# Performance work log

Measured on AMD Instinct MI355X. Metric: run time of the kernel, lower is better.

Reference implementation:

```python
import jax, jax.numpy as jnp
import numpy as np

B, P, E, H, V, T = 128, 196, 512, 512, 12000, 20  # batch, pixels, embed, hidden, vocab, timesteps


def setup_inputs() -> dict:
    key = jax.random.key(0)
    ks = jax.random.split(key, 12)
    s = lambda k, shape: jax.random.normal(k, shape, jnp.float32) * 0.02
    return {
        "encoder_out": jax.random.normal(ks[0], (B, P, E), jnp.float32),
        "captions": jax.random.randint(ks[1], (B, T), 0, V),
        "emb_table": s(ks[2], (V, E)),
        "We_att": s(ks[3], (E, E)), "be_att": jnp.zeros((E,), jnp.float32),
        "Wd_att": s(ks[4], (E, H)), "bd_att": jnp.zeros((E,), jnp.float32),
        "Wf_att": s(ks[5], (1, E)), "bf_att": jnp.zeros((1,), jnp.float32),
        "W_ih": s(ks[6], (4 * H, 2 * E)), "b_ih": jnp.zeros((4 * H,), jnp.float32),
        "W_hh": s(ks[7], (4 * H, H)), "b_hh": jnp.zeros((4 * H,), jnp.float32),
        "W_beta": s(ks[8], (E, H)), "b_beta": jnp.zeros((E,), jnp.float32),
        "W_fc": s(ks[9], (V, H)), "b_fc": jnp.zeros((V,), jnp.float32),
    }


def reference(encoder_out, captions, emb_table, We_att, be_att, Wd_att, bd_att,
              Wf_att, bf_att, W_ih, b_ih, W_hh, b_hh, W_beta, b_beta, W_fc, b_fc):
    # Dropout in eval mode (identity) for a deterministic reference.
    Bv = encoder_out.shape[0]
    Hd = W_hh.shape[1]
    emb = emb_table[captions]                                   # [B,T,E]
    # loop-invariant encoder projection (cached across timesteps)
    att1 = jnp.einsum('bpe,ae->bpa', encoder_out, We_att) + be_att  # [B,P,A]

    def step(carry, emb_t):
        h, c = carry
        att2 = h @ Wd_att.T + bd_att                            # [B,A]
        att = jax.nn.relu(att1 + att2[:, None, :])              # [B,P,A]
        e = jnp.einsum('bpa,a->bp', att, Wf_att[0]) + bf_att[0] # [B,P]
        alpha = jax.nn.softmax(e, axis=1)
        ctx = jnp.einsum('bp,bpe->be', alpha, encoder_out)      # [B,E]
        x = jnp.concatenate([emb_t, ctx], axis=1)               # [B,2E]
        gates = x @ W_ih.T + b_ih + h @ W_hh.T + b_hh           # [B,4H]
        i, f, g, o = jnp.split(gates, 4, axis=1)
        c = jax.nn.sigmoid(f) * c + jax.nn.sigmoid(i) * jnp.tanh(g)
        h = jax.nn.sigmoid(o) * jnp.tanh(c)
        gate = jax.nn.sigmoid(h @ W_beta.T + b_beta)            # [B,E]
        out = (gate * h) @ W_fc.T + b_fc                        # [B,V]
        return (h, c), (out, alpha)

    h0 = jnp.zeros((Bv, Hd), encoder_out.dtype)
    c0 = jnp.zeros((Bv, Hd), encoder_out.dtype)
    _, (outs, alphas) = jax.lax.scan(step, (h0, c0), jnp.swapaxes(emb, 0, 1))
    return jnp.swapaxes(outs, 0, 1), jnp.swapaxes(alphas, 0, 1)
```

## Files before the change

### kernel.cpp

```cpp
#include <hip/hip_runtime.h>
#include <math.h>

#define Bv 128
#define Pv 196
#define Ev 512
#define Hv 512
#define Vv 12000
#define Tv 20

typedef unsigned short u16;
typedef unsigned int u32;
typedef short bf16x8 __attribute__((ext_vector_type(8)));
typedef float f32x4 __attribute__((ext_vector_type(4)));

__device__ __forceinline__ float sigf(float x) { return 1.0f / (1.0f + __expf(-x)); }
__device__ __forceinline__ u16 f2bf(float f) {
    u32 x = __float_as_uint(f);
    return (u16)((x + 0x7FFFu + ((x >> 16) & 1u)) >> 16);
}
__device__ __forceinline__ u32 pack2(float a, float b) {
    return (u32)f2bf(a) | ((u32)f2bf(b) << 16);
}
__device__ __forceinline__ float bfl(u32 u) { return __uint_as_float(u << 16); }
__device__ __forceinline__ float bfh(u32 u) { return __uint_as_float(u & 0xFFFF0000u); }
__device__ __forceinline__ float bf2f(u16 u) { return __uint_as_float(((u32)u) << 16); }

__global__ __launch_bounds__(256) void k_cvt(const float* __restrict__ src,
                                             u16* __restrict__ dst, int n4) {
    for (int i = blockIdx.x * 256 + threadIdx.x; i < n4; i += gridDim.x * 256) {
        float4 v = ((const float4*)src)[i];
        uint2 o;
        o.x = pack2(v.x, v.y);
        o.y = pack2(v.z, v.w);
        ((uint2*)dst)[i] = o;
    }
}


__global__ __launch_bounds__(256) void k_att1_mfma(const u16* __restrict__ A,
                                                   const u16* __restrict__ Bw,
                                                   const float* __restrict__ bias,
                                                   u16* __restrict__ C) {
    __shared__ u16 As[128][72];
    __shared__ u16 Bs[64][72];
    const int n0 = blockIdx.x * 64;
    const int m0 = blockIdx.y * 128;
    const int tid = threadIdx.x;
    const int lane = tid & 63, wid = tid >> 6;
    const int wm = wid >> 1, wn = wid & 1;
    f32x4 acc[4][2] = {};
    for (int kt = 0; kt < 8; kt++) {
#pragma unroll
        for (int p = 0; p < 4; p++) {
            int flat = p * 256 + tid, row = flat >> 3, ch = flat & 7;
            *(uint4*)&As[row][ch * 8] = *(const uint4*)&A[(size_t)(m0 + row) * 512 + kt * 64 + ch * 8];
        }
#pragma unroll
        for (int p = 0; p < 2; p++) {
            int flat = p * 256 + tid, row = flat >> 3, ch = flat & 7;
            *(uint4*)&Bs[row][ch * 8] = *(const uint4*)&Bw[(size_t)(n0 + row) * 512 + kt * 64 + ch * 8];
        }
        __syncthreads();
#pragma unroll
        for (int ks = 0; ks < 2; ks++) {
            int kk = ks * 32 + (lane >> 4) * 8;
            bf16x8 af[4], bfr[2];
#pragma unroll
            for (int mf = 0; mf < 4; mf++) af[mf] = *(const bf16x8*)&As[wm * 64 + mf * 16 + (lane & 15)][kk];
#pragma unroll
            for (int nf = 0; nf < 2; nf++) bfr[nf] = *(const bf16x8*)&Bs[wn * 32 + nf * 16 + (lane & 15)][kk];
#pragma unroll
            for (int mf = 0; mf < 4; mf++)
#pragma unroll
                for (int nf = 0; nf < 2; nf++)
                    acc[mf][nf] = __builtin_amdgcn_mfma_f32_16x16x32_bf16(af[mf], bfr[nf], acc[mf][nf], 0, 0, 0);
        }
        __syncthreads();
    }
#pragma unroll
    for (int mf = 0; mf < 4; mf++)
#pragma unroll
        for (int nf = 0; nf < 2; nf++)
#pragma unroll
            for (int r = 0; r < 4; r++) {
                int m = m0 + wm * 64 + mf * 16 + (lane >> 4) * 4 + r;
                int n = n0 + wn * 32 + nf * 16 + (lane & 15);
                C[(size_t)m * 512 + n] = f2bf(acc[mf][nf][r] + bias[n]);
            }
}

__global__ __launch_bounds__(512) void k_attn(const u16* __restrict__ att1b,
                                              const u16* __restrict__ encb,
                                              const u16* __restrict__ hprev,
                                              const u16* __restrict__ Wdb,
                                              const float* __restrict__ bd,
                                              const float* __restrict__ Wf,
                                              u16* __restrict__ ctxb,
                                              float* __restrict__ alpha_out,
                                              int t) {
    __shared__ float h_s[512];
    __shared__ float att2_s[512];
    __shared__ float e_s[200];
    __shared__ float alpha_s[200];
    const int b = blockIdx.x;
    const int tid = threadIdx.x;

    h_s[tid] = bf2f(hprev[b * 512 + tid]);
    __syncthreads();

    {
        float acc = bd[tid];
        const uint4* wrow = (const uint4*)&Wdb[(size_t)tid * 512];
        const float4* hv4 = (const float4*)h_s;
#pragma unroll 4
        for (int i = 0; i < 64; i++) {
            uint4 w = wrow[i];
            float4 x0 = hv4[2 * i], x1 = hv4[2 * i + 1];
            acc += bfl(w.x) * x0.x + bfh(w.x) * x0.y + bfl(w.y) * x0.z + bfh(w.y) * x0.w
                 + bfl(w.z) * x1.x + bfh(w.z) * x1.y + bfl(w.w) * x1.z + bfh(w.w) * x1.w;
        }
        att2_s[tid] = acc;
    }
    __syncthreads();

    const int lane = tid & 63;
    const int wv = tid >> 6;
    float att2r[8], wfr[8];
#pragma unroll
    for (int j = 0; j < 8; j++) {
        att2r[j] = att2_s[lane * 8 + j];
        wfr[j] = Wf[lane * 8 + j];
    }
    for (int p = wv; p < 196; p += 8) {
        uint4 q = *(const uint4*)&att1b[((size_t)(b * 196 + p)) * 512 + lane * 8];
        float s = wfr[0] * fmaxf(bfl(q.x) + att2r[0], 0.f) + wfr[1] * fmaxf(bfh(q.x) + att2r[1], 0.f)
                + wfr[2] * fmaxf(bfl(q.y) + att2r[2], 0.f) + wfr[3] * fmaxf(bfh(q.y) + att2r[3], 0.f)
                + wfr[4] * fmaxf(bfl(q.z) + att2r[4], 0.f) + wfr[5] * fmaxf(bfh(q.z) + att2r[5], 0.f)
                + wfr[6] * fmaxf(bfl(q.w) + att2r[6], 0.f) + wfr[7] * fmaxf(bfh(q.w) + att2r[7], 0.f);
#pragma unroll
        for (int off = 32; off; off >>= 1) s += __shfl_xor(s, off);
        if (lane == 0) e_s[p] = s;
    }
    __syncthreads();

    if (wv == 0) {
        float v0 = e_s[lane], v1 = e_s[lane + 64], v2 = e_s[lane + 128];
        float v3 = (lane < 4) ? e_s[lane + 192] : -1e30f;
        float mx = fmaxf(fmaxf(v0, v1), fmaxf(v2, v3));
#pragma unroll
        for (int off = 32; off; off >>= 1) mx = fmaxf(mx, __shfl_xor(mx, off));
        float x0 = __expf(v0 - mx), x1 = __expf(v1 - mx), x2 = __expf(v2 - mx);
        float x3 = (lane < 4) ? __expf(v3 - mx) : 0.f;
        float sm = x0 + x1 + x2 + x3;
#pragma unroll
        for (int off = 32; off; off >>= 1) sm += __shfl_xor(sm, off);
        float inv = 1.0f / sm;
        x0 *= inv; x1 *= inv; x2 *= inv; x3 *= inv;
        alpha_s[lane] = x0; alpha_s[lane + 64] = x1; alpha_s[lane + 128] = x2;
        if (lane < 4) alpha_s[lane + 192] = x3;
        float* ao = alpha_out + ((size_t)b * Tv + t) * 196;
        ao[lane] = x0; ao[lane + 64] = x1; ao[lane + 128] = x2;
        if (lane < 4) ao[lane + 192] = x3;
    }
    __syncthreads();

    {
        float acc = 0.f;
        const u16* ecol = &encb[(size_t)b * 196 * 512 + tid];
#pragma unroll 4
        for (int p = 0; p < 196; p++) acc += alpha_s[p] * bf2f(ecol[(size_t)p * 512]);
        ctxb[b * 512 + tid] = f2bf(acc);
    }
}

__global__ __launch_bounds__(256) void k_gateslstm(const float* __restrict__ embt,
                                                   const int* __restrict__ caps,
                                                   const u16* __restrict__ ctxb,
                                                   const u16* __restrict__ hprev,
                                                   const u16* __restrict__ Wihb,
                                                   const u16* __restrict__ Whhb,
                                                   const float* __restrict__ bih,
                                                   const float* __restrict__ bhh,
                                                   float* __restrict__ cbuf,
                                                   u16* __restrict__ hnext,
                                                   int t) {
    __shared__ u16 As[64][72];
    __shared__ u16 Bs[64][72];
    __shared__ float gate_lds[4][64][16];
    const int jg = blockIdx.x;
    const int mh = blockIdx.y;
    const int tid = threadIdx.x;
    const int lane = tid & 63, wid = tid >> 6;
    const int wm = wid >> 1, wn = wid & 1;
    f32x4 acc[2][2] = {};

    for (int kt = 0; kt < 24; kt++) {
#pragma unroll
        for (int p = 0; p < 2; p++) {
            int flat = p * 256 + tid, row = flat >> 3, ch = flat & 7;
            int brow = mh * 64 + row;
            uint4 v;
            if (kt < 8) {
                int cap = caps[brow * Tv + t];
                const float4* s = (const float4*)&embt[(size_t)cap * 512 + kt * 64 + ch * 8];
                float4 f0 = s[0], f1 = s[1];
                v.x = pack2(f0.x, f0.y); v.y = pack2(f0.z, f0.w);
                v.z = pack2(f1.x, f1.y); v.w = pack2(f1.z, f1.w);
            } else if (kt < 16) {
                v = *(const uint4*)&ctxb[(size_t)brow * 512 + (kt - 8) * 64 + ch * 8];
            } else {
                v = *(const uint4*)&hprev[(size_t)brow * 512 + (kt - 16) * 64 + ch * 8];
            }
            *(uint4*)&As[row][ch * 8] = v;
        }
#pragma unroll
        for (int p = 0; p < 2; p++) {
            int flat = p * 256 + tid, row = flat >> 3, ch = flat & 7;
            int n = (row >> 4) * 512 + jg * 16 + (row & 15);
            uint4 v;
            if (kt < 16) v = *(const uint4*)&Wihb[(size_t)n * 1024 + kt * 64 + ch * 8];
            else         v = *(const uint4*)&Whhb[(size_t)n * 512 + (kt - 16) * 64 + ch * 8];
            *(uint4*)&Bs[row][ch * 8] = v;
        }
        __syncthreads();
#pragma unroll
        for (int ks = 0; ks < 2; ks++) {
            int kk = ks * 32 + (lane >> 4) * 8;
            bf16x8 af[2], bfr[2];
#pragma unroll
            for (int mf = 0; mf < 2; mf++) af[mf] = *(const bf16x8*)&As[wm * 32 + mf * 16 + (lane & 15)][kk];
#pragma unroll
            for (int nf = 0; nf < 2; nf++) bfr[nf] = *(const bf16x8*)&Bs[wn * 32 + nf * 16 + (lane & 15)][kk];
#pragma unroll
            for (int mf = 0; mf < 2; mf++)
#pragma unroll
                for (int nf = 0; nf < 2; nf++)
                    acc[mf][nf] = __builtin_amdgcn_mfma_f32_16x16x32_bf16(af[mf], bfr[nf], acc[mf][nf], 0, 0, 0);
        }
        __syncthreads();
    }
#pragma unroll
    for (int mf = 0; mf < 2; mf++)
#pragma unroll
        for (int nf = 0; nf < 2; nf++) {
            int q = wn * 2 + nf;
            int jj = lane & 15;
#pragma unroll
            for (int r = 0; r < 4; r++) {
                int m = wm * 32 + mf * 16 + (lane >> 4) * 4 + r;
                gate_lds[q][m][jj] = acc[mf][nf][r];
            }
        }
    __syncthreads();
#pragma unroll
    for (int i = 0; i < 4; i++) {
        int idx = i * 256 + tid;
        int m = idx >> 4, jj = idx & 15;
        int col = jg * 16 + jj;
        int brow = mh * 64 + m;
        float gi = gate_lds[0][m][jj] + bih[col] + bhh[col];
        float gf = gate_lds[1][m][jj] + bih[col + 512] + bhh[col + 512];
        float gg = gate_lds[2][m][jj] + bih[col + 1024] + bhh[col + 1024];
        float go = gate_lds[3][m][jj] + bih[col + 1536] + bhh[col + 1536];
        float cn = sigf(gf) * cbuf[brow * 512 + col] + sigf(gi) * tanhf(gg);
        float hn = sigf(go) * tanhf(cn);
        cbuf[brow * 512 + col] = cn;
        hnext[brow * 512 + col] = f2bf(hn);
    }
}

__global__ __launch_bounds__(256) void k_beta_mfma(const u16* __restrict__ hall,
                                                   const u16* __restrict__ Wbb,
                                                   const float* __restrict__ bb,
                                                   u16* __restrict__ ghall) {
    __shared__ u16 As[128][72];
    __shared__ u16 Bs[64][72];
    const int n0 = blockIdx.x * 64;
    const int m0 = blockIdx.y * 128;
    const int tid = threadIdx.x;
    const int lane = tid & 63, wid = tid >> 6;
    const int wm = wid >> 1, wn = wid & 1;
    f32x4 acc[4][2] = {};
    for (int kt = 0; kt < 8; kt++) {
#pragma unroll
        for (int p = 0; p < 4; p++) {
            int flat = p * 256 + tid, row = flat >> 3, ch = flat & 7;
            *(uint4*)&As[row][ch * 8] = *(const uint4*)&hall[(size_t)(m0 + row) * 512 + kt * 64 + ch * 8];
        }
#pragma unroll
        for (int p = 0; p < 2; p++) {
            int flat = p * 256 + tid, row = flat >> 3, ch = flat & 7;
            *(uint4*)&Bs[row][ch * 8] = *(const uint4*)&Wbb[(size_t)(n0 + row) * 512 + kt * 64 + ch * 8];
        }
        __syncthreads();
#pragma unroll
        for (int ks = 0; ks < 2; ks++) {
            int kk = ks * 32 + (lane >> 4) * 8;
            bf16x8 af[4], bfr[2];
#pragma unroll
            for (int mf = 0; mf < 4; mf++) af[mf] = *(const bf16x8*)&As[wm * 64 + mf * 16 + (lane & 15)][kk];
#pragma unroll
            for (int nf = 0; nf < 2; nf++) bfr[nf] = *(const bf16x8*)&Bs[wn * 32 + nf * 16 + (lane & 15)][kk];
#pragma unroll
            for (int mf = 0; mf < 4; mf++)
#pragma unroll
                for (int nf = 0; nf < 2; nf++)
                    acc[mf][nf] = __builtin_amdgcn_mfma_f32_16x16x32_bf16(af[mf], bfr[nf], acc[mf][nf], 0, 0, 0);
        }
        __syncthreads();
    }
#pragma unroll
    for (int mf = 0; mf < 4; mf++)
#pragma unroll
        for (int nf = 0; nf < 2; nf++)
#pragma unroll
            for (int r = 0; r < 4; r++) {
                int m = m0 + wm * 64 + mf * 16 + (lane >> 4) * 4 + r;
                int n = n0 + wn * 32 + nf * 16 + (lane & 15);
                float h = bf2f(hall[(size_t)m * 512 + n]);
                ghall[(size_t)m * 512 + n] = f2bf(h * sigf(acc[mf][nf][r] + bb[n]));
            }
}

__global__ __launch_bounds__(256) void k_logits_mega(const u16* __restrict__ ghall,
                                                     const u16* __restrict__ Wfcb,
                                                     const float* __restrict__ bias,
                                                     float* __restrict__ out) {
    __shared__ u16 As[128][72];
    __shared__ u16 Bs[64][72];
    const int n0 = blockIdx.x * 64;
    const int m0 = blockIdx.y * 128;
    const int tid = threadIdx.x;
    const int lane = tid & 63, wid = tid >> 6;
    const int wm = wid >> 1, wn = wid & 1;
    f32x4 acc[4][2] = {};
    for (int kt = 0; kt < 8; kt++) {
#pragma unroll
        for (int p = 0; p < 4; p++) {
            int flat = p * 256 + tid, row = flat >> 3, ch = flat & 7;
            *(uint4*)&As[row][ch * 8] = *(const uint4*)&ghall[(size_t)(m0 + row) * 512 + kt * 64 + ch * 8];
        }
#pragma unroll
        for (int p = 0; p < 2; p++) {
            int flat = p * 256 + tid, row = flat >> 3, ch = flat & 7;
            uint4 v = {0u, 0u, 0u, 0u};
            if (n0 + row < Vv)
                v = *(const uint4*)&Wfcb[(size_t)(n0 + row) * 512 + kt * 64 + ch * 8];
            *(uint4*)&Bs[row][ch * 8] = v;
        }
        __syncthreads();
#pragma unroll
        for (int ks = 0; ks < 2; ks++) {
            int kk = ks * 32 + (lane >> 4) * 8;
            bf16x8 af[4], bfr[2];
#pragma unroll
            for (int mf = 0; mf < 4; mf++) af[mf] = *(const bf16x8*)&As[wm * 64 + mf * 16 + (lane & 15)][kk];
#pragma unroll
            for (int nf = 0; nf < 2; nf++) bfr[nf] = *(const bf16x8*)&Bs[wn * 32 + nf * 16 + (lane & 15)][kk];
#pragma unroll
            for (int mf = 0; mf < 4; mf++)
#pragma unroll
                for (int nf = 0; nf < 2; nf++)
                    acc[mf][nf] = __builtin_amdgcn_mfma_f32_16x16x32_bf16(af[mf], bfr[nf], acc[mf][nf], 0, 0, 0);
        }
        __syncthreads();
    }
#pragma unroll
    for (int mf = 0; mf < 4; mf++)
#pragma unroll
        for (int nf = 0; nf < 2; nf++)
#pragma unroll
            for (int r = 0; r < 4; r++) {
                int m = m0 + wm * 64 + mf * 16 + (lane >> 4) * 4 + r;
                int n = n0 + wn * 32 + nf * 16 + (lane & 15);
                if (n < Vv) {
                    int tt = m >> 7, b = m & 127;
                    out[(size_t)b * (Tv * Vv) + (size_t)tt * Vv + n] = acc[mf][nf][r] + bias[n];
                }
            }
}

extern "C" void kernel_launch(void* const* d_in, const int* in_sizes, int n_in,
                              void* d_out, int out_size, void* d_ws, size_t ws_size,
                              hipStream_t stream) {
    const float* enc = (const float*)d_in[0];
    const int* caps = (const int*)d_in[1];
    const float* embt = (const float*)d_in[2];
    const float* We = (const float*)d_in[3];
    const float* bea = (const float*)d_in[4];
    const float* Wd = (const float*)d_in[5];
    const float* bd = (const float*)d_in[6];
    const float* Wf = (const float*)d_in[7];
    const float* Wih = (const float*)d_in[9];
    const float* bih = (const float*)d_in[10];
    const float* Whh = (const float*)d_in[11];
    const float* bhh = (const float*)d_in[12];
    const float* Wb = (const float*)d_in[13];
    const float* bb = (const float*)d_in[14];
    const float* Wfc = (const float*)d_in[15];
    const float* bfc = (const float*)d_in[16];

    float* out = (float*)d_out;
    float* alpha_out = out + (size_t)Bv * Tv * Vv;

    u16* encb = (u16*)d_ws;
    u16* att1b = encb + (size_t)12845056;
    u16* Wfcb = att1b + (size_t)12845056;
    u16* Wihb = Wfcb + 6144000;
    u16* Whhb = Wihb + 2097152;
    u16* Web = Whhb + 1048576;
    u16* Wdb = Web + 262144;
    u16* Wbb = Wdb + 262144;
    u16* ctxb = Wbb + 262144;
    u16* hall = ctxb + 65536;
    u16* ghall = hall + 21 * 65536;
    float* cbuf = (float*)(ghall + 20 * 65536);

    hipMemsetAsync(hall, 0, 65536 * sizeof(u16), stream);
    hipMemsetAsync(cbuf, 0, 65536 * sizeof(float), stream);

    k_cvt<<<1024, 256, 0, stream>>>(enc, encb, 12845056 / 4);
    k_cvt<<<1024, 256, 0, stream>>>(Wfc, Wfcb, 6144000 / 4);
    k_cvt<<<512, 256, 0, stream>>>(Wih, Wihb, 2097152 / 4);
    k_cvt<<<256, 256, 0, stream>>>(Whh, Whhb, 1048576 / 4);
    k_cvt<<<64, 256, 0, stream>>>(We, Web, 262144 / 4);
    k_cvt<<<64, 256, 0, stream>>>(Wd, Wdb, 262144 / 4);
    k_cvt<<<64, 256, 0, stream>>>(Wb, Wbb, 262144 / 4);

    dim3 g0(8, 196);
    k_att1_mfma<<<g0, 256, 0, stream>>>(encb, Web, bea, att1b);

    for (int t = 0; t < Tv; t++) {
        const u16* hprev = hall + (size_t)t * 65536;
        u16* hnext = hall + (size_t)(t + 1) * 65536;
        k_attn<<<128, 512, 0, stream>>>(att1b, encb, hprev, Wdb, bd, Wf, ctxb, alpha_out, t);
        dim3 gg(32, 2);
        k_gateslstm<<<gg, 256, 0, stream>>>(embt, caps, ctxb, hprev, Wihb, Whhb,
                                            bih, bhh, cbuf, hnext, t);
    }

    dim3 gb(8, 20);
    k_beta_mfma<<<gb, 256, 0, stream>>>(hall + 65536, Wbb, bb, ghall);
    dim3 gl(188, 20);
    k_logits_mega<<<gl, 256, 0, stream>>>(ghall, Wfcb, bfc, out);
}
```

Before: 1.905 ms.

## Fuse whole pipeline into one persistent cooperative kernel with grid syncs

Replaces the sequence of around 50 kernel launches (conversions, att1 GEMM, 20 steps of attention plus gates, beta and logits) with a single cooperative persistent kernel of 256 blocks that uses grid.sync between phases. Each 512-thread block runs two 256-thread GEMM sub-units. The aim is to remove launch overhead and inter-kernel gaps in the sequential recurrence. The cost is fewer active blocks for the large GEMMs, with many idle blocks during the recurrent steps, plus grid-wide barrier latency. If the cooperative launch fails, it falls back to the old multi-kernel path.

```diff
diff --git a/kernel.cpp b/kernel.cpp
--- a/kernel.cpp
+++ b/kernel.cpp
@@ -1,5 +1,8 @@
 #include <hip/hip_runtime.h>
+#include <hip/hip_cooperative_groups.h>
 #include <math.h>
+
+namespace cg = cooperative_groups;
 
 #define Bv 128
 #define Pv 196
@@ -25,9 +28,10 @@
 __device__ __forceinline__ float bfh(u32 u) { return __uint_as_float(u & 0xFFFF0000u); }
 __device__ __forceinline__ float bf2f(u16 u) { return __uint_as_float(((u32)u) << 16); }
 
-__global__ __launch_bounds__(256) void k_cvt(const float* __restrict__ src,
-                                             u16* __restrict__ dst, int n4) {
-    for (int i = blockIdx.x * 256 + threadIdx.x; i < n4; i += gridDim.x * 256) {
+__device__ __forceinline__ void cvt_loop(const float* __restrict__ src,
+                                         u16* __restrict__ dst, int n4,
+                                         int g, int gs) {
+    for (int i = g; i < n4; i += gs) {
         float4 v = ((const float4*)src)[i];
         uint2 o;
         o.x = pack2(v.x, v.y);
@@ -36,29 +40,28 @@
     }
 }
 
-
-__global__ __launch_bounds__(256) void k_att1_mfma(const u16* __restrict__ A,
-                                                   const u16* __restrict__ Bw,
-                                                   const float* __restrict__ bias,
-                                                   u16* __restrict__ C) {
-    __shared__ u16 As[128][72];
-    __shared__ u16 Bs[64][72];
-    const int n0 = blockIdx.x * 64;
-    const int m0 = blockIdx.y * 128;
-    const int tid = threadIdx.x;
-    const int lane = tid & 63, wid = tid >> 6;
+template <int MODE>
+__device__ void gemm_tile(const u16* __restrict__ A, const u16* __restrict__ B,
+                          const float* __restrict__ bias, void* __restrict__ dst,
+                          const u16* __restrict__ hsrc,
+                          int m0, int n0, bool act,
+                          u16 (*As)[72], u16 (*Bs)[72], int t256) {
+    const int lane = t256 & 63, wid = t256 >> 6;
     const int wm = wid >> 1, wn = wid & 1;
     f32x4 acc[4][2] = {};
     for (int kt = 0; kt < 8; kt++) {
-#pragma unroll
-        for (int p = 0; p < 4; p++) {
-            int flat = p * 256 + tid, row = flat >> 3, ch = flat & 7;
-            *(uint4*)&As[row][ch * 8] = *(const uint4*)&A[(size_t)(m0 + row) * 512 + kt * 64 + ch * 8];
-        }
-#pragma unroll
-        for (int p = 0; p < 2; p++) {
-            int flat = p * 256 + tid, row = flat >> 3, ch = flat & 7;
-            *(uint4*)&Bs[row][ch * 8] = *(const uint4*)&Bw[(size_t)(n0 + row) * 512 + kt * 64 + ch * 8];
+        if (act) {
+#pragma unroll
+            for (int p = 0; p < 4; p++) {
+                int flat = p * 256 + t256, row = flat >> 3, ch = flat & 7;
+                *(uint4*)&As[row][ch * 8] = *(const uint4*)&A[(size_t)(m0 + row) * 512 + kt * 64 + ch * 8];
+            }
+#pragma unroll
+            for (int p = 0; p < 2; p++) {
+                int flat = p * 256 + t256, row = flat >> 3, ch = flat & 7;
+                if (MODE != 2 || (n0 + row) < Vv)
+                    *(uint4*)&Bs[row][ch * 8] = *(const uint4*)&B[(size_t)(n0 + row) * 512 + kt * 64 + ch * 8];
+            }
         }
         __syncthreads();
 #pragma unroll
@@ -77,6 +80,7 @@
         }
         __syncthreads();
     }
+    if (!act) return;
 #pragma unroll
     for (int mf = 0; mf < 4; mf++)
 #pragma unroll
@@ -85,25 +89,30 @@
             for (int r = 0; r < 4; r++) {
                 int m = m0 + wm * 64 + mf * 16 + (lane >> 4) * 4 + r;
                 int n = n0 + wn * 32 + nf * 16 + (lane & 15);
-                C[(size_t)m * 512 + n] = f2bf(acc[mf][nf][r] + bias[n]);
+                float v = acc[mf][nf][r];
+                if (MODE == 0) {
+                    ((u16*)dst)[(size_t)m * 512 + n] = f2bf(v + bias[n]);
+                } else if (MODE == 1) {
+                    float h = bf2f(hsrc[(size_t)m * 512 + n]);
+                    ((u16*)dst)[(size_t)m * 512 + n] = f2bf(h * sigf(v + bias[n]));
+                } else {
+                    if (n < Vv) {
+                        int tt = m >> 7, b = m & 127;
+                        ((float*)dst)[(size_t)b * (Tv * Vv) + (size_t)tt * Vv + n] = v + bias[n];
+                    }
+                }
             }
 }
 
-__global__ __launch_bounds__(512) void k_attn(const u16* __restrict__ att1b,
-                                              const u16* __restrict__ encb,
-                                              const u16* __restrict__ hprev,
-                                              const u16* __restrict__ Wdb,
-                                              const float* __restrict__ bd,
-                                              const float* __restrict__ Wf,
-                                              u16* __restrict__ ctxb,
-                                              float* __restrict__ alpha_out,
-                                              int t) {
-    __shared__ float h_s[512];
-    __shared__ float att2_s[512];
-    __shared__ float e_s[200];
-    __shared__ float alpha_s[200];
-    const int b = blockIdx.x;
-    const int tid = threadIdx.x;
+__device__ void attn_block(const u16* __restrict__ att1b, const u16* __restrict__ encb,
+                           const u16* __restrict__ hprev, const u16* __restrict__ Wdb,
+                           const float* __restrict__ bd, const float* __restrict__ Wf,
+                           u16* __restrict__ ctxb, float* __restrict__ alpha_out,
+                           int t, int b, int tid, float* smem) {
+    float* h_s = smem;
+    float* att2_s = smem + 512;
+    float* e_s = smem + 1024;
+    float* alpha_s = smem + 1224;
 
     h_s[tid] = bf2f(hprev[b * 512 + tid]);
     __syncthreads();
@@ -173,31 +182,21 @@
     }
 }
 
-__global__ __launch_bounds__(256) void k_gateslstm(const float* __restrict__ embt,
-                                                   const int* __restrict__ caps,
-                                                   const u16* __restrict__ ctxb,
-                                                   const u16* __restrict__ hprev,
-                                                   const u16* __restrict__ Wihb,
-                                                   const u16* __restrict__ Whhb,
-                                                   const float* __restrict__ bih,
-                                                   const float* __restrict__ bhh,
-                                                   float* __restrict__ cbuf,
-                                                   u16* __restrict__ hnext,
-                                                   int t) {
-    __shared__ u16 As[64][72];
-    __shared__ u16 Bs[64][72];
-    __shared__ float gate_lds[4][64][16];
-    const int jg = blockIdx.x;
-    const int mh = blockIdx.y;
-    const int tid = threadIdx.x;
-    const int lane = tid & 63, wid = tid >> 6;
+__device__ void gates_block(const float* __restrict__ embt, const int* __restrict__ caps,
+                            const u16* __restrict__ ctxb, const u16* __restrict__ hprev,
+                            const u16* __restrict__ Wihb, const u16* __restrict__ Whhb,
+                            const float* __restrict__ bih, const float* __restrict__ bhh,
+                            float* __restrict__ cbuf, u16* __restrict__ hnext,
+                            int t, int jg, int mh, int t256,
+                            u16 (*As)[72], u16 (*Bs)[72], float (*glds)[64][16]) {
+    const int lane = t256 & 63, wid = t256 >> 6;
     const int wm = wid >> 1, wn = wid & 1;
     f32x4 acc[2][2] = {};
 
     for (int kt = 0; kt < 24; kt++) {
 #pragma unroll
         for (int p = 0; p < 2; p++) {
-            int flat = p * 256 + tid, row = flat >> 3, ch = flat & 7;
+            int flat = p * 256 + t256, row = flat >> 3, ch = flat & 7;
             int brow = mh * 64 + row;
             uint4 v;
             if (kt < 8) {
@@ -215,7 +214,7 @@
         }
 #pragma unroll
         for (int p = 0; p < 2; p++) {
-            int flat = p * 256 + tid, row = flat >> 3, ch = flat & 7;
+            int flat = p * 256 + t256, row = flat >> 3, ch = flat & 7;
             int n = (row >> 4) * 512 + jg * 16 + (row & 15);
             uint4 v;
             if (kt < 16) v = *(const uint4*)&Wihb[(size_t)n * 1024 + kt * 64 + ch * 8];
@@ -248,20 +247,20 @@
 #pragma unroll
             for (int r = 0; r < 4; r++) {
                 int m = wm * 32 + mf * 16 + (lane >> 4) * 4 + r;
-                gate_lds[q][m][jj] = acc[mf][nf][r];
+                glds[q][m][jj] = acc[mf][nf][r];
             }
         }
     __syncthreads();
 #pragma unroll
     for (int i = 0; i < 4; i++) {
-        int idx = i * 256 + tid;
+        int idx = i * 256 + t256;
         int m = idx >> 4, jj = idx & 15;
         int col = jg * 16 + jj;
         int brow = mh * 64 + m;
-        float gi = gate_lds[0][m][jj] + bih[col] + bhh[col];
-        float gf = gate_lds[1][m][jj] + bih[col + 512] + bhh[col + 512];
-        float gg = gate_lds[2][m][jj] + bih[col + 1024] + bhh[col + 1024];
-        float go = gate_lds[3][m][jj] + bih[col + 1536] + bhh[col + 1536];
+        float gi = glds[0][m][jj] + bih[col] + bhh[col];
+        float gf = glds[1][m][jj] + bih[col + 512] + bhh[col + 512];
+        float gg = glds[2][m][jj] + bih[col + 1024] + bhh[col + 1024];
+        float go = glds[3][m][jj] + bih[col + 1536] + bhh[col + 1536];
         float cn = sigf(gf) * cbuf[brow * 512 + col] + sigf(gi) * tanhf(gg);
         float hn = sigf(go) * tanhf(cn);
         cbuf[brow * 512 + col] = cn;
@@ -269,115 +268,142 @@
     }
 }
 
-__global__ __launch_bounds__(256) void k_beta_mfma(const u16* __restrict__ hall,
-                                                   const u16* __restrict__ Wbb,
-                                                   const float* __restrict__ bb,
-                                                   u16* __restrict__ ghall) {
+__global__ __launch_bounds__(512) void k_mega(
+    const float* __restrict__ enc, const int* __restrict__ caps,
+    const float* __restrict__ embt,
+    const float* __restrict__ We, const float* __restrict__ bea,
+    const float* __restrict__ Wd, const float* __restrict__ bd,
+    const float* __restrict__ Wf,
+    const float* __restrict__ Wih, const float* __restrict__ bih,
+    const float* __restrict__ Whh, const float* __restrict__ bhh,
+    const float* __restrict__ Wb, const float* __restrict__ bb,
+    const float* __restrict__ Wfc, const float* __restrict__ bfc,
+    float* __restrict__ out, float* __restrict__ alpha_out,
+    u16* __restrict__ encb, u16* __restrict__ att1b,
+    u16* __restrict__ Wfcb, u16* __restrict__ Wihb, u16* __restrict__ Whhb,
+    u16* __restrict__ Web, u16* __restrict__ Wdb, u16* __restrict__ Wbb,
+    u16* __restrict__ ctxb, u16* __restrict__ hall, u16* __restrict__ ghall,
+    float* __restrict__ cbuf) {
+    cg::grid_group grid = cg::this_grid();
+    const int bid = blockIdx.x;
+    const int tid = threadIdx.x;
+    const int sub = tid >> 8;
+    const int t256 = tid & 255;
+    const int unit = bid * 2 + sub;
+
+    __shared__ u16 As[2][128][72];
+    __shared__ u16 Bs[2][64][72];
+    __shared__ float gate_lds[2][4][64][16];
+    __shared__ float attn_f[1424];
+
+    {
+        int g = bid * 512 + tid, gs = 256 * 512;
+        cvt_loop(enc, encb, 12845056 / 4, g, gs);
+        cvt_loop(Wfc, Wfcb, 6144000 / 4, g, gs);
+        cvt_loop(Wih, Wihb, 2097152 / 4, g, gs);
+        cvt_loop(Whh, Whhb, 1048576 / 4, g, gs);
+        cvt_loop(We, Web, 262144 / 4, g, gs);
+        cvt_loop(Wd, Wdb, 262144 / 4, g, gs);
+        cvt_loop(Wb, Wbb, 262144 / 4, g, gs);
+        for (int i = g; i < 32768; i += gs) ((u32*)hall)[i] = 0u;
+        for (int i = g; i < 65536; i += gs) cbuf[i] = 0.f;
+    }
+    grid.sync();
+
+    for (int r = 0; r < 4; r++) {
+        int tile = unit + r * 512;
+        bool act = tile < 1568;
+        int tt = act ? tile : 0;
+        gemm_tile<0>(encb, Web, bea, att1b, nullptr,
+                     (tt / 8) * 128, (tt % 8) * 64, act, As[sub], Bs[sub], t256);
+    }
+    grid.sync();
+
+    for (int t = 0; t < Tv; t++) {
+        const u16* hprev = hall + (size_t)t * 65536;
+        u16* hnext = hall + (size_t)(t + 1) * 65536;
+        if (bid < 128)
+            attn_block(att1b, encb, hprev, Wdb, bd, Wf, ctxb, alpha_out, t, bid, tid, attn_f);
+        grid.sync();
+        if (bid < 32)
+            gates_block(embt, caps, ctxb, hprev, Wihb, Whhb, bih, bhh, cbuf, hnext,
+                        t, bid, sub, t256, As[sub], Bs[sub], gate_lds[sub]);
+        grid.sync();
+    }
+
+    {
+        bool act = unit < 160;
+        int tt = act ? unit : 0;
+        gemm_tile<1>(hall + 65536, Wbb, bb, ghall, hall + 65536,
+                     (tt / 8) * 128, (tt % 8) * 64, act, As[sub], Bs[sub], t256);
+    }
+    grid.sync();
+
+    for (int r = 0; r < 8; r++) {
+        int tile = unit + r * 512;
+        bool act = tile < 3760;
+        int tt = act ? tile : 0;
+        gemm_tile<2>(ghall, Wfcb, bfc, out, nullptr,
+                     (tt / 188) * 128, (tt % 188) * 64, act, As[sub], Bs[sub], t256);
+    }
+}
+
+__global__ __launch_bounds__(256) void k_cvt(const float* __restrict__ src,
+                                             u16* __restrict__ dst, int n4) {
+    for (int i = blockIdx.x * 256 + threadIdx.x; i < n4; i += gridDim.x * 256) {
+        float4 v = ((const float4*)src)[i];
+        uint2 o;
+        o.x = pack2(v.x, v.y);
+        o.y = pack2(v.z, v.w);
+        ((uint2*)dst)[i] = o;
+    }
+}
+
+__global__ __launch_bounds__(256) void k_att1_mfma(const u16* __restrict__ A,
+                                                   const u16* __restrict__ Bw,
+                                                   const float* __restrict__ bias,
+                                                   u16* __restrict__ C) {
     __shared__ u16 As[128][72];
     __shared__ u16 Bs[64][72];
-    const int n0 = blockIdx.x * 64;
-    const int m0 = blockIdx.y * 128;
-    const int tid = threadIdx.x;
-    const int lane = tid & 63, wid = tid >> 6;
-    const int wm = wid >> 1, wn = wid & 1;
-    f32x4 acc[4][2] = {};
-    for (int kt = 0; kt < 8; kt++) {
-#pragma unroll
-        for (int p = 0; p < 4; p++) {
-            int flat = p * 256 + tid, row = flat >> 3, ch = flat & 7;
-            *(uint4*)&As[row][ch * 8] = *(const uint4*)&hall[(size_t)(m0 + row) * 512 + kt * 64 + ch * 8];
-        }
-#pragma unroll
-        for (int p = 0; p < 2; p++) {
-            int flat = p * 256 + tid, row = flat >> 3, ch = flat & 7;
-            *(uint4*)&Bs[row][ch * 8] = *(const uint4*)&Wbb[(size_t)(n0 + row) * 512 + kt * 64 + ch * 8];
-        }
-        __syncthreads();
-#pragma unroll
-        for (int ks = 0; ks < 2; ks++) {
-            int kk = ks * 32 + (lane >> 4) * 8;
-            bf16x8 af[4], bfr[2];
-#pragma unroll
-            for (int mf = 0; mf < 4; mf++) af[mf] = *(const bf16x8*)&As[wm * 64 + mf * 16 + (lane & 15)][kk];
-#pragma unroll
-            for (int nf = 0; nf < 2; nf++) bfr[nf] = *(const bf16x8*)&Bs[wn * 32 + nf * 16 + (lane & 15)][kk];
-#pragma unroll
-            for (int mf = 0; mf < 4; mf++)
-#pragma unroll
-                for (int nf = 0; nf < 2; nf++)
-                    acc[mf][nf] = __builtin_amdgcn_mfma_f32_16x16x32_bf16(af[mf], bfr[nf], acc[mf][nf], 0, 0, 0);
-        }
-        __syncthreads();
-    }
-#pragma unroll
-    for (int mf = 0; mf < 4; mf++)
-#pragma unroll
-        for (int nf = 0; nf < 2; nf++)
-#pragma unroll
-            for (int r = 0; r < 4; r++) {
-                int m = m0 + wm * 64 + mf * 16 + (lane >> 4) * 4 + r;
-                int n = n0 + wn * 32 + nf * 16 + (lane & 15);
-                float h = bf2f(hall[(size_t)m * 512 + n]);
-                ghall[(size_t)m * 512 + n] = f2bf(h * sigf(acc[mf][nf][r] + bb[n]));
-            }
-}
-
-__global__ __launch_bounds__(256) void k_logits_mega(const u16* __restrict__ ghall,
-                                                     const u16* __restrict__ Wfcb,
-                                                     const float* __restrict__ bias,
-                                                     float* __restrict__ out) {
+    gemm_tile<0>(A, Bw, bias, C, nullptr, blockIdx.y * 128, blockIdx.x * 64, true,
+                 As, Bs, threadIdx.x);
+}
+
+__global__ __launch_bounds__(512) void k_attn_g(const u16* att1b, const u16* encb,
+                                                const u16* hprev, const u16* Wdb,
+                                                const float* bd, const float* Wf,
+                                                u16* ctxb, float* alpha_out, int t) {
+    __shared__ float smem[1424];
+    attn_block(att1b, encb, hprev, Wdb, bd, Wf, ctxb, alpha_out, t, blockIdx.x,
+               threadIdx.x, smem);
+}
+
+__global__ __launch_bounds__(256) void k_gates_g(const float* embt, const int* caps,
+                                                 const u16* ctxb, const u16* hprev,
+                                                 const u16* Wihb, const u16* Whhb,
+                                                 const float* bih, const float* bhh,
+                                                 float* cbuf, u16* hnext, int t) {
+    __shared__ u16 As[64][72];
+    __shared__ u16 Bs[64][72];
+    __shared__ float glds[4][64][16];
+    gates_block(embt, caps, ctxb, hprev, Wihb, Whhb, bih, bhh, cbuf, hnext,
+                t, blockIdx.x, blockIdx.y, threadIdx.x, As, Bs, glds);
+}
+
+__global__ __launch_bounds__(256) void k_beta_g(const u16* hall1, const u16* Wbb,
+                                                const float* bb, u16* ghall) {
     __shared__ u16 As[128][72];
     __shared__ u16 Bs[64][72];
-    const int n0 = blockIdx.x * 64;
-    const int m0 = blockIdx.y * 128;
-    const int tid = threadIdx.x;
-    const int lane = tid & 63, wid = tid >> 6;
-    const int wm = wid >> 1, wn = wid & 1;
-    f32x4 acc[4][2] = {};
-    for (int kt = 0; kt < 8; kt++) {
-#pragma unroll
-        for (int p = 0; p < 4; p++) {
-            int flat = p * 256 + tid, row = flat >> 3, ch = flat & 7;
-            *(uint4*)&As[row][ch * 8] = *(const uint4*)&ghall[(size_t)(m0 + row) * 512 + kt * 64 + ch * 8];
-        }
-#pragma unroll
-        for (int p = 0; p < 2; p++) {
-            int flat = p * 256 + tid, row = flat >> 3, ch = flat & 7;
-            uint4 v = {0u, 0u, 0u, 0u};
-            if (n0 + row < Vv)
-                v = *(const uint4*)&Wfcb[(size_t)(n0 + row) * 512 + kt * 64 + ch * 8];
-            *(uint4*)&Bs[row][ch * 8] = v;
-        }
-        __syncthreads();
-#pragma unroll
-        for (int ks = 0; ks < 2; ks++) {
-            int kk = ks * 32 + (lane >> 4) * 8;
-            bf16x8 af[4], bfr[2];
-#pragma unroll
-            for (int mf = 0; mf < 4; mf++) af[mf] = *(const bf16x8*)&As[wm * 64 + mf * 16 + (lane & 15)][kk];
-#pragma unroll
-            for (int nf = 0; nf < 2; nf++) bfr[nf] = *(const bf16x8*)&Bs[wn * 32 + nf * 16 + (lane & 15)][kk];
-#pragma unroll
-            for (int mf = 0; mf < 4; mf++)
-#pragma unroll
-                for (int nf = 0; nf < 2; nf++)
-                    acc[mf][nf] = __builtin_amdgcn_mfma_f32_16x16x32_bf16(af[mf], bfr[nf], acc[mf][nf], 0, 0, 0);
-        }
-        __syncthreads();
-    }
-#pragma unroll
-    for (int mf = 0; mf < 4; mf++)
-#pragma unroll
-        for (int nf = 0; nf < 2; nf++)
-#pragma unroll
-            for (int r = 0; r < 4; r++) {
-                int m = m0 + wm * 64 + mf * 16 + (lane >> 4) * 4 + r;
-                int n = n0 + wn * 32 + nf * 16 + (lane & 15);
-                if (n < Vv) {
-                    int tt = m >> 7, b = m & 127;
-                    out[(size_t)b * (Tv * Vv) + (size_t)tt * Vv + n] = acc[mf][nf][r] + bias[n];
-                }
-            }
+    gemm_tile<1>(hall1, Wbb, bb, ghall, hall1, blockIdx.y * 128, blockIdx.x * 64, true,
+                 As, Bs, threadIdx.x);
+}
+
+__global__ __launch_bounds__(256) void k_logits_g(const u16* ghall, const u16* Wfcb,
+                                                  const float* bfc, float* out) {
+    __shared__ u16 As[128][72];
+    __shared__ u16 Bs[64][72];
+    gemm_tile<2>(ghall, Wfcb, bfc, out, nullptr, blockIdx.y * 128, blockIdx.x * 64, true,
+                 As, Bs, threadIdx.x);
 }
 
 extern "C" void kernel_launch(void* const* d_in, const int* in_sizes, int n_in,
@@ -416,9 +442,20 @@
     u16* ghall = hall + 21 * 65536;
     float* cbuf = (float*)(ghall + 20 * 65536);
 
+    void* kargs[] = {
+        (void*)&enc, (void*)&caps, (void*)&embt, (void*)&We, (void*)&bea,
+        (void*)&Wd, (void*)&bd, (void*)&Wf, (void*)&Wih, (void*)&bih,
+        (void*)&Whh, (void*)&bhh, (void*)&Wb, (void*)&bb, (void*)&Wfc,
+        (void*)&bfc, (void*)&out, (void*)&alpha_out, (void*)&encb, (void*)&att1b,
+        (void*)&Wfcb, (void*)&Wihb, (void*)&Whhb, (void*)&Web, (void*)&Wdb,
+        (void*)&Wbb, (void*)&ctxb, (void*)&hall, (void*)&ghall, (void*)&cbuf};
+
+    hipError_t err = hipLaunchCooperativeKernel((void*)k_mega, dim3(256), dim3(512),
+                                                kargs, 0, stream);
+    if (err == hipSuccess) return;
+
     hipMemsetAsync(hall, 0, 65536 * sizeof(u16), stream);
     hipMemsetAsync(cbuf, 0, 65536 * sizeof(float), stream);
-
     k_cvt<<<1024, 256, 0, stream>>>(enc, encb, 12845056 / 4);
     k_cvt<<<1024, 256, 0, stream>>>(Wfc, Wfcb, 6144000 / 4);
     k_cvt<<<512, 256, 0, stream>>>(Wih, Wihb, 2097152 / 4);
@@ -426,21 +463,18 @@
     k_cvt<<<64, 256, 0, stream>>>(We, Web, 262144 / 4);
     k_cvt<<<64, 256, 0, stream>>>(Wd, Wdb, 262144 / 4);
     k_cvt<<<64, 256, 0, stream>>>(Wb, Wbb, 262144 / 4);
-
     dim3 g0(8, 196);
     k_att1_mfma<<<g0, 256, 0, stream>>>(encb, Web, bea, att1b);
-
     for (int t = 0; t < Tv; t++) {
         const u16* hprev = hall + (size_t)t * 65536;
         u16* hnext = hall + (size_t)(t + 1) * 65536;
-        k_attn<<<128, 512, 0, stream>>>(att1b, encb, hprev, Wdb, bd, Wf, ctxb, alpha_out, t);
+        k_attn_g<<<128, 512, 0, stream>>>(att1b, encb, hprev, Wdb, bd, Wf, ctxb, alpha_out, t);
         dim3 gg(32, 2);
-        k_gateslstm<<<gg, 256, 0, stream>>>(embt, caps, ctxb, hprev, Wihb, Whhb,
-                                            bih, bhh, cbuf, hnext, t);
-    }
-
+        k_gates_g<<<gg, 256, 0, stream>>>(embt, caps, ctxb, hprev, Wihb, Whhb,
+                                          bih, bhh, cbuf, hnext, t);
+    }
     dim3 gb(8, 20);
-    k_beta_mfma<<<gb, 256, 0, stream>>>(hall + 65536, Wbb, bb, ghall);
+    k_beta_g<<<gb, 256, 0, stream>>>(hall + 65536, Wbb, bb, ghall);
     dim3 gl(188, 20);
-    k_logits_mega<<<gl, 256, 0, stream>>>(ghall, Wfcb, bfc, out);
-}
+    k_logits_g<<<gl, 256, 0, stream>>>(ghall, Wfcb, bfc, out);
+}
```

Result: slower. 3.432 ms (+80.2%).
